# Performance work log

Measured on AMD Instinct MI355X. Metric: run time of the kernel, lower is better.

## Reference

```python
import jax, jax.numpy as jnp
from jax import lax
import numpy as np

EPS = 1e-12  # torch F.normalize eps


def setup_inputs() -> dict:
    key = jax.random.key(0)
    ks = jax.random.split(key, 5)
    B, C, H, W = 8, 192, 128, 128
    heads = 4
    x = jax.random.normal(ks[0], (B, C, H, W), dtype=jnp.float32)
    qkv_w = jax.random.normal(ks[1], (3 * C, C), dtype=jnp.float32) * (1.0 / np.sqrt(C))
    dw_w = jax.random.normal(ks[2], (3 * C, 1, 3, 3), dtype=jnp.float32) * (1.0 / 3.0)
    proj_w = jax.random.normal(ks[3], (C, C), dtype=jnp.float32) * (1.0 / np.sqrt(C))
    temperature = jnp.ones((1, heads, 1, 1), dtype=jnp.float32)
    return {"x": x, "qkv_w": qkv_w, "dw_w": dw_w, "proj_w": proj_w,
            "temperature": temperature, "num_heads": heads}


def _l2_normalize(t):
    # matches torch F.normalize(dim=-1): x / max(||x||, eps)
    n = jnp.sqrt(jnp.sum(t * t, axis=-1, keepdims=True))
    return t / jnp.maximum(n, EPS)


def reference(x, qkv_w, dw_w, proj_w, temperature, num_heads):
    b, c, h, w = x.shape
    # 1x1 conv (no bias) == channel GEMM
    qkv = jnp.einsum('oc,bchw->bohw', qkv_w, x)
    # 3x3 depthwise conv, padding=1, groups=3c
    qkv = lax.conv_general_dilated(
        qkv, dw_w, window_strides=(1, 1), padding='SAME',
        feature_group_count=3 * c,
        dimension_numbers=('NCHW', 'OIHW', 'NCHW'))
    q, k, v = jnp.split(qkv, 3, axis=1)
    hw = h * w
    dh = c // num_heads  # per-head channel dim
    q = q.reshape(b, num_heads, dh, hw)
    k = k.reshape(b, num_heads, dh, hw)
    v = v.reshape(b, num_heads, dh, hw)
    q = _l2_normalize(q)
    k = _l2_normalize(k)
    # channel attention: [b, heads, dh, dh]
    attn = jnp.einsum('bhcn,bhdn->bhcd', q, k) * temperature
    attn = jax.nn.softmax(attn, axis=-1)
    out = jnp.einsum('bhcd,bhdn->bhcn', attn, v).reshape(b, c, h, w)
    out = jnp.einsum('oc,bchw->bohw', proj_w, out)
    return out
```

## Files before the change

kernel.cpp:

```cpp
#include <hip/hip_runtime.h>
#include <hip/hip_bf16.h>

#define CIN 192
#define C3 576
#define HWPX 16384
#define NHEADS 4
#define DH 48

typedef unsigned short ushort_t;
typedef __attribute__((ext_vector_type(8))) short bf16x8;
typedef __attribute__((ext_vector_type(4))) float f32x4;

__device__ __forceinline__ float bf2f(unsigned short u) {
    return __uint_as_float(((unsigned int)u) << 16);
}
__device__ __forceinline__ unsigned short f2bf(float f) {
    unsigned int u = __float_as_uint(f);
    unsigned int r = (u >> 16) & 1u;
    u += 0x7fffu + r;
    return (unsigned short)(u >> 16);
}
__device__ __forceinline__ void up8(uint4 a, float* o) {
    o[0] = __uint_as_float(a.x << 16); o[1] = __uint_as_float(a.x & 0xffff0000u);
    o[2] = __uint_as_float(a.y << 16); o[3] = __uint_as_float(a.y & 0xffff0000u);
    o[4] = __uint_as_float(a.z << 16); o[5] = __uint_as_float(a.z & 0xffff0000u);
    o[6] = __uint_as_float(a.w << 16); o[7] = __uint_as_float(a.w & 0xffff0000u);
}

#define ASYNC_COPY16(gptr, lptr)                                                   \
    __builtin_amdgcn_global_load_lds(                                              \
        (__attribute__((address_space(1))) void*)(gptr),                           \
        (__attribute__((address_space(3))) void*)(lptr), 16, 0, 0)

__global__ __launch_bounds__(256) void k_cvtw(const float* __restrict__ w,
                                              ushort_t* __restrict__ wb) {
    int i = (blockIdx.x * 256 + threadIdx.x) * 4;
    float4 v = *(const float4*)(w + i);
    uint2 pk;
    pk.x = (unsigned)f2bf(v.x) | ((unsigned)f2bf(v.y) << 16);
    pk.y = (unsigned)f2bf(v.z) | ((unsigned)f2bf(v.w) << 16);
    *(uint2*)(wb + i) = pk;
}

__global__ __launch_bounds__(512) void k_gemm(const float* __restrict__ A,
                                              const ushort_t* __restrict__ B,
                                              ushort_t* __restrict__ C) {
    __shared__ ushort_t sA[2][128 * 32];
    __shared__ ushort_t sB[2][192 * 32];
    const int t = threadIdx.x;
    const int lane = t & 63, wave = t >> 6;
    const int wrow = wave >> 1, wcol = wave & 1;
    const int pix0 = blockIdx.x * 128;
    const int o0 = blockIdx.y * 192;
    const int b = blockIdx.z;
    const ushort_t* Bb = B + (size_t)o0 * CIN;

    const int cc = t >> 4;
    const int jj = t & 15;

    float avf[8];
    auto loadA = [&](int kc) {
        const float* Ab = A + (size_t)b * CIN * HWPX +
                          (size_t)(kc + cc) * HWPX + pix0 + jj;
#pragma unroll
        for (int i = 0; i < 8; ++i) avf[i] = Ab[16 * i];
    };
    auto writeA = [&](int buf) {
        ushort_t* s = sA[buf];
#pragma unroll
        for (int i = 0; i < 8; ++i) {
            int row = jj + 16 * i;
            int slot = ((cc >> 3) + (row >> 1) + (row >> 3)) & 3;
            s[row * 32 + slot * 8 + (cc & 7)] = f2bf(avf[i]);
        }
    };
    auto stageB = [&](int buf, int kc) {
        {
            int row = t >> 2, slot = t & 3;
            int g = (slot + (row >> 1)) & 3;
            const ushort_t* gp = Bb + (size_t)row * CIN + kc + g * 8;
            ushort_t* lp = &sB[buf][(wave * 64) * 8];
            ASYNC_COPY16(gp, lp);
        }
        if (t < 256) {
            int e = 512 + t;
            int row = e >> 2, slot = e & 3;
            int g = (slot + (row >> 1)) & 3;
            const ushort_t* gp = Bb + (size_t)row * CIN + kc + g * 8;
            ushort_t* lp = &sB[buf][(512 + wave * 64) * 8];
            ASYNC_COPY16(gp, lp);
        }
    };

    f32x4 acc[2][6];
#pragma unroll
    for (int mi = 0; mi < 2; ++mi)
#pragma unroll
        for (int ni = 0; ni < 6; ++ni) acc[mi][ni] = (f32x4){0.f, 0.f, 0.f, 0.f};

    loadA(0);
    writeA(0);
    stageB(0, 0);
#pragma unroll
    for (int ks = 0; ks < 6; ++ks) {
        __syncthreads();
        const int buf = ks & 1;
        if (ks < 5) {
            loadA((ks + 1) * 32);
            stageB(buf ^ 1, (ks + 1) * 32);
        }
        const ushort_t* a_ = sA[buf];
        const ushort_t* b_ = sB[buf];
        const int c = lane >> 4;
        bf16x8 af[2], bfr[6];
#pragma unroll
        for (int mi = 0; mi < 2; ++mi) {
            int row = wrow * 32 + mi * 16 + (lane & 15);
            int slot = (c + (row >> 1) + (row >> 3)) & 3;
            af[mi] = *(const bf16x8*)&a_[row * 32 + slot * 8];
        }
#pragma unroll
        for (int ni = 0; ni < 6; ++ni) {
            int row = wcol * 96 + ni * 16 + (lane & 15);
            int slot = (c - (row >> 1)) & 3;
            bfr[ni] = *(const bf16x8*)&b_[row * 32 + slot * 8];
        }
#pragma unroll
        for (int mi = 0; mi < 2; ++mi)
#pragma unroll
            for (int ni = 0; ni < 6; ++ni)
                acc[mi][ni] = __builtin_amdgcn_mfma_f32_16x16x32_bf16(
                    af[mi], bfr[ni], acc[mi][ni], 0, 0, 0);
        if (ks < 5) writeA(buf ^ 1);
    }

    const int ocol = lane & 15;
    const int prow = (lane >> 4) * 4;
#pragma unroll
    for (int mi = 0; mi < 2; ++mi) {
        int pix = pix0 + wrow * 32 + mi * 16 + prow;
#pragma unroll
        for (int ni = 0; ni < 6; ++ni) {
            int o = o0 + wcol * 96 + ni * 16 + ocol;
            f32x4 v = acc[mi][ni];
            ushort_t* Cp = C + ((size_t)b * C3 + o) * HWPX + pix;
            uint2 pk;
            pk.x = (unsigned)f2bf(v[0]) | ((unsigned)f2bf(v[1]) << 16);
            pk.y = (unsigned)f2bf(v[2]) | ((unsigned)f2bf(v[3]) << 16);
            *(uint2*)Cp = pk;
        }
    }
}

__global__ __launch_bounds__(256, 1) void k_gramdw(const ushort_t* __restrict__ pre,
                                                   const float* __restrict__ dww,
                                                   float* __restrict__ gpart,
                                                   float* __restrict__ normp) {
    __shared__ char smem[NHEADS * DH * DH * 4];
    ushort_t* sCw = (ushort_t*)smem + (threadIdx.x >> 6) * (96 * 40);
    float* sG = (float*)smem;

    const int chunk = blockIdx.x, h = blockIdx.y, b = blockIdx.z;
    const int t = threadIdx.x;
    const int lane = t & 63, wave = t >> 6;
    const int y0 = chunk * 16;

    const ushort_t* plane[3];
    float wreg[3][9];
    int pxb[3];
#pragma unroll
    for (int u = 0; u < 3; ++u) {
        int id = lane + 64 * u;
        int c96 = id >> 1;
        int gch = (c96 < DH) ? (h * DH + c96) : (CIN + h * DH + (c96 - DH));
        plane[u] = pre + ((size_t)b * C3 + gch) * HWPX;
        pxb[u] = wave * 32 + (id & 1) * 16;
#pragma unroll
        for (int k = 0; k < 9; ++k) wreg[u][k] = dww[gch * 9 + k];
    }

    float ssq[3] = {0.f, 0.f, 0.f};
    f32x4 acc[3][3];
#pragma unroll
    for (int i = 0; i < 3; ++i)
#pragma unroll
        for (int j = 0; j < 3; ++j) acc[i][j] = (f32x4){0.f, 0.f, 0.f, 0.f};

    uint4 ring[3][3][2];
    ushort_t lfr[3][3], rgr[3][3];
    uint4 nx[3][2];
    ushort_t nlf[3], nrg[3];

    auto LOADROW = [&](int YY) {
#pragma unroll
        for (int u = 0; u < 3; ++u) {
            bool ok = ((unsigned)YY < 128u);
            const ushort_t* rp = plane[u] + YY * 128 + pxb[u];
            if (ok) {
                nx[u][0] = *(const uint4*)rp;
                nx[u][1] = *(const uint4*)(rp + 8);
                nlf[u] = (pxb[u] > 0) ? rp[-1] : (ushort_t)0;
                nrg[u] = (pxb[u] + 16 < 128) ? rp[16] : (ushort_t)0;
            } else {
                nx[u][0] = make_uint4(0, 0, 0, 0);
                nx[u][1] = make_uint4(0, 0, 0, 0);
                nlf[u] = 0;
                nrg[u] = 0;
            }
        }
    };
    auto PUT = [&](int rp) {
#pragma unroll
        for (int u = 0; u < 3; ++u) {
            ring[rp][u][0] = nx[u][0];
            ring[rp][u][1] = nx[u][1];
            lfr[rp][u] = nlf[u];
            rgr[rp][u] = nrg[u];
        }
    };

    LOADROW(y0 - 1); PUT(0);
    LOADROW(y0);     PUT(1);
    LOADROW(y0 + 1); PUT(2);

    for (int s = 0; s < 16; ++s) {
        if (s < 15) LOADROW(y0 + s + 2);
#pragma unroll
        for (int u = 0; u < 3; ++u) {
            int id = lane + 64 * u;
            float in[3][18];
#pragma unroll
            for (int r = 0; r < 3; ++r) {
                in[r][0] = bf2f(lfr[r][u]);
                up8(ring[r][u][0], &in[r][1]);
                up8(ring[r][u][1], &in[r][9]);
                in[r][17] = bf2f(rgr[r][u]);
            }
            unsigned pk[8];
#pragma unroll
            for (int j2 = 0; j2 < 8; ++j2) {
                float o0 = 0.f, o1 = 0.f;
#pragma unroll
                for (int ky = 0; ky < 3; ++ky) {
                    o0 = fmaf(wreg[u][ky * 3 + 0], in[ky][2 * j2 + 0], o0);
                    o0 = fmaf(wreg[u][ky * 3 + 1], in[ky][2 * j2 + 1], o0);
                    o0 = fmaf(wreg[u][ky * 3 + 2], in[ky][2 * j2 + 2], o0);
                    o1 = fmaf(wreg[u][ky * 3 + 0], in[ky][2 * j2 + 1], o1);
                    o1 = fmaf(wreg[u][ky * 3 + 1], in[ky][2 * j2 + 2], o1);
                    o1 = fmaf(wreg[u][ky * 3 + 2], in[ky][2 * j2 + 3], o1);
                }
                ssq[u] = fmaf(o0, o0, ssq[u]);
                ssq[u] = fmaf(o1, o1, ssq[u]);
                pk[j2] = (unsigned)f2bf(o0) | ((unsigned)f2bf(o1) << 16);
            }
            uint4* dst = (uint4*)&sCw[(id >> 1) * 40 + ((id & 1) << 4)];
            dst[0] = make_uint4(pk[0], pk[1], pk[2], pk[3]);
            dst[1] = make_uint4(pk[4], pk[5], pk[6], pk[7]);
        }
        {
            bf16x8 af[3], bk[3];
#pragma unroll
            for (int i = 0; i < 3; ++i)
                af[i] = *(const bf16x8*)&sCw[(i * 16 + (lane & 15)) * 40 + (lane >> 4) * 8];
#pragma unroll
            for (int j = 0; j < 3; ++j)
                bk[j] = *(const bf16x8*)&sCw[(48 + j * 16 + (lane & 15)) * 40 + (lane >> 4) * 8];
#pragma unroll
            for (int i = 0; i < 3; ++i)
#pragma unroll
                for (int j = 0; j < 3; ++j)
                    acc[i][j] = __builtin_amdgcn_mfma_f32_16x16x32_bf16(af[i], bk[j],
                                                                        acc[i][j], 0, 0, 0);
        }
        if (s < 15) {
#pragma unroll
            for (int u = 0; u < 3; ++u) {
                ring[0][u][0] = ring[1][u][0]; ring[0][u][1] = ring[1][u][1];
                ring[1][u][0] = ring[2][u][0]; ring[1][u][1] = ring[2][u][1];
                ring[2][u][0] = nx[u][0];      ring[2][u][1] = nx[u][1];
                lfr[0][u] = lfr[1][u]; lfr[1][u] = lfr[2][u]; lfr[2][u] = nlf[u];
                rgr[0][u] = rgr[1][u]; rgr[1][u] = rgr[2][u]; rgr[2][u] = nrg[u];
            }
        }
    }

    __syncthreads();
    const int crow = (lane >> 4) * 4;
    const int dcol = lane & 15;
#pragma unroll
    for (int i = 0; i < 3; ++i)
#pragma unroll
        for (int j = 0; j < 3; ++j)
#pragma unroll
            for (int r = 0; r < 4; ++r)
                sG[(size_t)wave * DH * DH + (i * 16 + crow + r) * DH + j * 16 + dcol] =
                    acc[i][j][r];
    __syncthreads();
    float* g = gpart + (((size_t)(b * NHEADS + h)) * 8 + chunk) * (DH * DH);
    for (int e = t; e < DH * DH; e += 256)
        g[e] = sG[e] + sG[DH * DH + e] + sG[2 * DH * DH + e] + sG[3 * DH * DH + e];

    float* np = normp + ((((size_t)(b * NHEADS + h)) * 8 + chunk) * 4 + wave) * 192;
#pragma unroll
    for (int u = 0; u < 3; ++u) np[lane + 64 * u] = ssq[u];
}

__global__ __launch_bounds__(256) void k_attn(const float* __restrict__ gpart,
                                              const float* __restrict__ normp,
                                              const float* __restrict__ temperature,
                                              float* __restrict__ att) {
    __shared__ float sA[DH][DH + 1];
    __shared__ float nrm[96];
    const int h = blockIdx.x, b = blockIdx.y;
    const int t = threadIdx.x;
    const size_t bh = b * NHEADS + h;
    if (t < 96) {
        float s = 0.f;
        for (int ck = 0; ck < 8; ++ck)
#pragma unroll
            for (int w = 0; w < 4; ++w) {
                const float* np = normp + ((bh * 8 + ck) * 4 + w) * 192 + t * 2;
                s += np[0] + np[1];
            }
        nrm[t] = fmaxf(sqrtf(s), 1e-12f);
    }
    __syncthreads();
    const float* base = gpart + (bh * 8) * (DH * DH);
    for (int e = t; e < DH * DH; e += 256) {
        float s = 0.f;
#pragma unroll
        for (int c8 = 0; c8 < 8; ++c8) s += base[(size_t)c8 * DH * DH + e];
        int c = e / DH, d = e % DH;
        sA[c][d] = s / (nrm[c] * nrm[48 + d]) * temperature[h];
    }
    __syncthreads();
    if (t < DH) {
        float m = -1e30f;
#pragma unroll
        for (int d = 0; d < DH; ++d) m = fmaxf(m, sA[t][d]);
        float s = 0.f;
        float row[DH];
#pragma unroll
        for (int d = 0; d < DH; ++d) {
            row[d] = expf(sA[t][d] - m);
            s += row[d];
        }
        float inv = 1.f / s;
#pragma unroll
        for (int d = 0; d < DH; ++d) sA[t][d] = row[d] * inv;
    }
    __syncthreads();
    float* ob = att + bh * DH * DH;
    for (int e = t; e < DH * DH; e += 256) ob[e] = sA[e / DH][e % DH];
}

__global__ __launch_bounds__(256) void k_mw(const float* __restrict__ att,
                                            const float* __restrict__ proj_w,
                                            ushort_t* __restrict__ Mw) {
    __shared__ float satt[NHEADS][DH][DH];
    __shared__ float sproj[32][CIN];
    const int o0 = blockIdx.x * 32, b = blockIdx.y;
    const int t = threadIdx.x;
    {
        const float4* src = (const float4*)(att + (size_t)b * NHEADS * DH * DH);
        float4* dst = (float4*)&satt[0][0][0];
        for (int e = t; e < NHEADS * DH * DH / 4; e += 256) dst[e] = src[e];
        const float4* ps = (const float4*)(proj_w + (size_t)o0 * CIN);
        float4* pd = (float4*)&sproj[0][0];
        for (int e = t; e < 32 * CIN / 4; e += 256) pd[e] = ps[e];
    }
    __syncthreads();
    ushort_t* ob = Mw + (size_t)b * CIN * CIN + (size_t)o0 * CIN;
    for (int e = t; e < 32 * CIN; e += 256) {
        int o = e / CIN, dg = e % CIN;
        int h = dg / DH, d = dg % DH;
        float s = 0.f;
#pragma unroll
        for (int c = 0; c < DH; ++c) s = fmaf(sproj[o][h * DH + c], satt[h][c][d], s);
        ob[e] = f2bf(s);
    }
}

__global__ __launch_bounds__(512) void k_gemmv(const ushort_t* __restrict__ pre,
                                               const float* __restrict__ dww,
                                               const ushort_t* __restrict__ B,
                                               float* __restrict__ C) {
    __shared__ ushort_t sA[2][128 * 32];
    __shared__ ushort_t sB[2][192 * 32];
    const int t = threadIdx.x;
    const int lane = t & 63, wave = t >> 6;
    const int wrow = wave >> 1, wcol = wave & 1;
    const int Y = blockIdx.x;
    const int pix0 = Y * 128;
    const int b = blockIdx.z;
    const ushort_t* Bb = B + (size_t)b * CIN * CIN;

    const int cc = t >> 4;
    const int jj = t & 15;
    const int x0 = jj * 8;

    uint4 m[3];
    ushort_t l16[3], rg16[3];
    float wv[9];
    ushort_t av[8];

    auto loadV = [&](int kc) {
        int ch = kc + cc;
        const ushort_t* pl = pre + ((size_t)b * C3 + 2 * CIN + ch) * HWPX;
#pragma unroll
        for (int r = 0; r < 3; ++r) {
            int YY = Y - 1 + r;
            bool ok = ((unsigned)YY < 128u);
            const ushort_t* rp = pl + YY * 128;
            if (ok) {
                m[r] = *(const uint4*)(rp + x0);
                l16[r] = (x0 > 0) ? rp[x0 - 1] : (ushort_t)0;
                rg16[r] = (x0 < 120) ? rp[x0 + 8] : (ushort_t)0;
            } else {
                m[r] = make_uint4(0, 0, 0, 0);
                l16[r] = 0;
                rg16[r] = 0;
            }
        }
#pragma unroll
        for (int k = 0; k < 9; ++k) wv[k] = dww[(2 * CIN + ch) * 9 + k];
    };
    auto convV = [&]() {
        float in[3][10];
#pragma unroll
        for (int r = 0; r < 3; ++r) {
            in[r][0] = bf2f(l16[r]);
            up8(m[r], &in[r][1]);
            in[r][9] = bf2f(rg16[r]);
        }
#pragma unroll
        for (int j = 0; j < 8; ++j) {
            float o = 0.f;
#pragma unroll
            for (int ky = 0; ky < 3; ++ky) {
                o = fmaf(wv[ky * 3 + 0], in[ky][j + 0], o);
                o = fmaf(wv[ky * 3 + 1], in[ky][j + 1], o);
                o = fmaf(wv[ky * 3 + 2], in[ky][j + 2], o);
            }
            av[j] = f2bf(o);
        }
    };
    auto writeA = [&](int buf) {
        ushort_t* s = sA[buf];
#pragma unroll
        for (int i = 0; i < 8; ++i) {
            int row = jj * 8 + i;
            int slot = ((cc >> 3) + (row >> 1) + (row >> 3)) & 3;
            s[row * 32 + slot * 8 + (cc & 7)] = av[i];
        }
    };
    auto stageB = [&](int buf, int kc) {
        {
            int row = t >> 2, slot = t & 3;
            int g = (slot + (row >> 1)) & 3;
            const ushort_t* gp = Bb + (size_t)row * CIN + kc + g * 8;
            ushort_t* lp = &sB[buf][(wave * 64) * 8];
            ASYNC_COPY16(gp, lp);
        }
        if (t < 256) {
            int e = 512 + t;
            int row = e >> 2, slot = e & 3;
            int g = (slot + (row >> 1)) & 3;
            const ushort_t* gp = Bb + (size_t)row * CIN + kc + g * 8;
            ushort_t* lp = &sB[buf][(512 + wave * 64) * 8];
            ASYNC_COPY16(gp, lp);
        }
    };

    f32x4 acc[2][6];
#pragma unroll
    for (int mi = 0; mi < 2; ++mi)
#pragma unroll
        for (int ni = 0; ni < 6; ++ni) acc[mi][ni] = (f32x4){0.f, 0.f, 0.f, 0.f};

    loadV(0);
    convV();
    writeA(0);
    stageB(0, 0);
#pragma unroll
    for (int ks = 0; ks < 6; ++ks) {
        __syncthreads();
        const int buf = ks & 1;
        if (ks < 5) {
            loadV((ks + 1) * 32);
            stageB(buf ^ 1, (ks + 1) * 32);
        }
        const ushort_t* a_ = sA[buf];
        const ushort_t* b_ = sB[buf];
        const int c = lane >> 4;
        bf16x8 af[2], bfr[6];
#pragma unroll
        for (int mi = 0; mi < 2; ++mi) {
            int row = wrow * 32 + mi * 16 + (lane & 15);
            int slot = (c + (row >> 1) + (row >> 3)) & 3;
            af[mi] = *(const bf16x8*)&a_[row * 32 + slot * 8];
        }
#pragma unroll
        for (int ni = 0; ni < 6; ++ni) {
            int row = wcol * 96 + ni * 16 + (lane & 15);
            int slot = (c - (row >> 1)) & 3;
            bfr[ni] = *(const bf16x8*)&b_[row * 32 + slot * 8];
        }
#pragma unroll
        for (int mi = 0; mi < 2; ++mi)
#pragma unroll
            for (int ni = 0; ni < 6; ++ni)
                acc[mi][ni] = __builtin_amdgcn_mfma_f32_16x16x32_bf16(
                    af[mi], bfr[ni], acc[mi][ni], 0, 0, 0);
        if (ks < 5) {
            convV();
            writeA(buf ^ 1);
        }
    }

    const int ocol = lane & 15;
    const int prow = (lane >> 4) * 4;
#pragma unroll
    for (int mi = 0; mi < 2; ++mi) {
        int pix = pix0 + wrow * 32 + mi * 16 + prow;
#pragma unroll
        for (int ni = 0; ni < 6; ++ni) {
            int o = wcol * 96 + ni * 16 + ocol;
            f32x4 v = acc[mi][ni];
            float* Cp = C + ((size_t)b * CIN + o) * HWPX + pix;
            *(float4*)Cp = make_float4(v[0], v[1], v[2], v[3]);
        }
    }
}

extern "C" void kernel_launch(void* const* d_in, const int* in_sizes, int n_in,
                              void* d_out, int out_size, void* d_ws, size_t ws_size,
                              hipStream_t stream) {
    const float* x = (const float*)d_in[0];
    const float* qkv_w = (const float*)d_in[1];
    const float* dw_w = (const float*)d_in[2];
    const float* proj_w = (const float*)d_in[3];
    const float* temperature = (const float*)d_in[4];
    float* out = (float*)d_out;

    char* ws = (char*)d_ws;
    ushort_t* pre = (ushort_t*)ws;
    float* normp = (float*)(ws + 150994944);
    float* gpart = (float*)(ws + 151781376);
    ushort_t* Mw = (ushort_t*)(ws + 154140672);
    float* attb = (float*)(ws + 154730496);
    ushort_t* wq = (ushort_t*)(ws + 155025408);

    k_cvtw<<<dim3(108), 256, 0, stream>>>(qkv_w, wq);
    k_gemm<<<dim3(128, 3, 8), 512, 0, stream>>>(x, wq, pre);
    k_gramdw<<<dim3(8, NHEADS, 8), 256, 0, stream>>>(pre, dw_w, gpart, normp);
    k_attn<<<dim3(NHEADS, 8), 256, 0, stream>>>(gpart, normp, temperature, attb);
    k_mw<<<dim3(6, 8), 256, 0, stream>>>(attb, proj_w, Mw);
    k_gemmv<<<dim3(128, 1, 8), 512, 0, stream>>>(pre, dw_w, Mw, out);
}
```

Before: 225.1 us.

## Keep full input tile in LDS and loop over all output groups per block

```diff
diff --git a/kernel.cpp b/kernel.cpp
--- a/kernel.cpp
+++ b/kernel.cpp
@@ -45,36 +45,40 @@
 __global__ __launch_bounds__(512) void k_gemm(const float* __restrict__ A,
                                               const ushort_t* __restrict__ B,
                                               ushort_t* __restrict__ C) {
-    __shared__ ushort_t sA[2][128 * 32];
+    __shared__ ushort_t sA[6 * 128 * 32];
     __shared__ ushort_t sB[2][192 * 32];
     const int t = threadIdx.x;
     const int lane = t & 63, wave = t >> 6;
     const int wrow = wave >> 1, wcol = wave & 1;
     const int pix0 = blockIdx.x * 128;
-    const int o0 = blockIdx.y * 192;
     const int b = blockIdx.z;
-    const ushort_t* Bb = B + (size_t)o0 * CIN;
 
     const int cc = t >> 4;
     const int jj = t & 15;
 
-    float avf[8];
-    auto loadA = [&](int kc) {
-        const float* Ab = A + (size_t)b * CIN * HWPX +
-                          (size_t)(kc + cc) * HWPX + pix0 + jj;
-#pragma unroll
-        for (int i = 0; i < 8; ++i) avf[i] = Ab[16 * i];
-    };
-    auto writeA = [&](int buf) {
-        ushort_t* s = sA[buf];
-#pragma unroll
-        for (int i = 0; i < 8; ++i) {
-            int row = jj + 16 * i;
-            int slot = ((cc >> 3) + (row >> 1) + (row >> 3)) & 3;
-            s[row * 32 + slot * 8 + (cc & 7)] = f2bf(avf[i]);
-        }
-    };
-    auto stageB = [&](int buf, int kc) {
+    {
+        float avf[6][8];
+#pragma unroll
+        for (int c = 0; c < 6; ++c) {
+            const float* Ab = A + (size_t)b * CIN * HWPX +
+                              (size_t)(c * 32 + cc) * HWPX + pix0 + jj;
+#pragma unroll
+            for (int i = 0; i < 8; ++i) avf[c][i] = Ab[16 * i];
+        }
+#pragma unroll
+        for (int c = 0; c < 6; ++c) {
+            ushort_t* s = &sA[c * 4096];
+#pragma unroll
+            for (int i = 0; i < 8; ++i) {
+                int row = jj + 16 * i;
+                int slot = ((cc >> 3) + (row >> 1) + (row >> 3)) & 3;
+                s[row * 32 + slot * 8 + (cc & 7)] = f2bf(avf[c][i]);
+            }
+        }
+    }
+
+    auto stageB = [&](int buf, int og, int kc) {
+        const ushort_t* Bb = B + (size_t)og * 192 * CIN;
         {
             int row = t >> 2, slot = t & 3;
             int g = (slot + (row >> 1)) & 3;
@@ -98,56 +102,57 @@
 #pragma unroll
         for (int ni = 0; ni < 6; ++ni) acc[mi][ni] = (f32x4){0.f, 0.f, 0.f, 0.f};
 
-    loadA(0);
-    writeA(0);
-    stageB(0, 0);
-#pragma unroll
-    for (int ks = 0; ks < 6; ++ks) {
-        __syncthreads();
-        const int buf = ks & 1;
-        if (ks < 5) {
-            loadA((ks + 1) * 32);
-            stageB(buf ^ 1, (ks + 1) * 32);
-        }
-        const ushort_t* a_ = sA[buf];
-        const ushort_t* b_ = sB[buf];
-        const int c = lane >> 4;
-        bf16x8 af[2], bfr[6];
-#pragma unroll
-        for (int mi = 0; mi < 2; ++mi) {
-            int row = wrow * 32 + mi * 16 + (lane & 15);
-            int slot = (c + (row >> 1) + (row >> 3)) & 3;
-            af[mi] = *(const bf16x8*)&a_[row * 32 + slot * 8];
-        }
-#pragma unroll
-        for (int ni = 0; ni < 6; ++ni) {
-            int row = wcol * 96 + ni * 16 + (lane & 15);
-            int slot = (c - (row >> 1)) & 3;
-            bfr[ni] = *(const bf16x8*)&b_[row * 32 + slot * 8];
-        }
-#pragma unroll
-        for (int mi = 0; mi < 2; ++mi)
-#pragma unroll
-            for (int ni = 0; ni < 6; ++ni)
-                acc[mi][ni] = __builtin_amdgcn_mfma_f32_16x16x32_bf16(
-                    af[mi], bfr[ni], acc[mi][ni], 0, 0, 0);
-        if (ks < 5) writeA(buf ^ 1);
-    }
+    stageB(0, 0, 0);
 
     const int ocol = lane & 15;
     const int prow = (lane >> 4) * 4;
-#pragma unroll
-    for (int mi = 0; mi < 2; ++mi) {
-        int pix = pix0 + wrow * 32 + mi * 16 + prow;
-#pragma unroll
-        for (int ni = 0; ni < 6; ++ni) {
-            int o = o0 + wcol * 96 + ni * 16 + ocol;
-            f32x4 v = acc[mi][ni];
-            ushort_t* Cp = C + ((size_t)b * C3 + o) * HWPX + pix;
-            uint2 pk;
-            pk.x = (unsigned)f2bf(v[0]) | ((unsigned)f2bf(v[1]) << 16);
-            pk.y = (unsigned)f2bf(v[2]) | ((unsigned)f2bf(v[3]) << 16);
-            *(uint2*)Cp = pk;
+    const int c = lane >> 4;
+
+#pragma unroll
+    for (int og = 0; og < 3; ++og) {
+#pragma unroll
+        for (int ks = 0; ks < 6; ++ks) {
+            const int step = og * 6 + ks;
+            const int buf = step & 1;
+            __syncthreads();
+            if (step + 1 < 18)
+                stageB(buf ^ 1, (step + 1) / 6, ((step + 1) % 6) * 32);
+            const ushort_t* a_ = &sA[ks * 4096];
+            const ushort_t* b_ = sB[buf];
+            bf16x8 af[2], bfr[6];
+#pragma unroll
+            for (int mi = 0; mi < 2; ++mi) {
+                int row = wrow * 32 + mi * 16 + (lane & 15);
+                int slot = (c + (row >> 1) + (row >> 3)) & 3;
+                af[mi] = *(const bf16x8*)&a_[row * 32 + slot * 8];
+            }
+#pragma unroll
+            for (int ni = 0; ni < 6; ++ni) {
+                int row = wcol * 96 + ni * 16 + (lane & 15);
+                int slot = (c - (row >> 1)) & 3;
+                bfr[ni] = *(const bf16x8*)&b_[row * 32 + slot * 8];
+            }
+#pragma unroll
+            for (int mi = 0; mi < 2; ++mi)
+#pragma unroll
+                for (int ni = 0; ni < 6; ++ni)
+                    acc[mi][ni] = __builtin_amdgcn_mfma_f32_16x16x32_bf16(
+                        af[mi], bfr[ni], acc[mi][ni], 0, 0, 0);
+        }
+#pragma unroll
+        for (int mi = 0; mi < 2; ++mi) {
+            int pix = pix0 + wrow * 32 + mi * 16 + prow;
+#pragma unroll
+            for (int ni = 0; ni < 6; ++ni) {
+                int o = og * 192 + wcol * 96 + ni * 16 + ocol;
+                f32x4 v = acc[mi][ni];
+                ushort_t* Cp = C + ((size_t)b * C3 + o) * HWPX + pix;
+                uint2 pk;
+                pk.x = (unsigned)f2bf(v[0]) | ((unsigned)f2bf(v[1]) << 16);
+                pk.y = (unsigned)f2bf(v[2]) | ((unsigned)f2bf(v[3]) << 16);
+                *(uint2*)Cp = pk;
+                acc[mi][ni] = (f32x4){0.f, 0.f, 0.f, 0.f};
+            }
         }
     }
 }
@@ -552,7 +557,7 @@
     ushort_t* wq = (ushort_t*)(ws + 155025408);
 
     k_cvtw<<<dim3(108), 256, 0, stream>>>(qkv_w, wq);
-    k_gemm<<<dim3(128, 3, 8), 512, 0, stream>>>(x, wq, pre);
+    k_gemm<<<dim3(128, 1, 8), 512, 0, stream>>>(x, wq, pre);
     k_gramdw<<<dim3(8, NHEADS, 8), 256, 0, stream>>>(pre, dw_w, gpart, normp);
     k_attn<<<dim3(NHEADS, 8), 256, 0, stream>>>(gpart, normp, temperature, attb);
     k_mw<<<dim3(6, 8), 256, 0, stream>>>(attb, proj_w, Mw);
```

Measured after the change: 212.7 us. 5.5% less time.
